# Optimization experiments

Measured on AMD Instinct MI355X. Metric: run time of the kernel, lower is better.

Reference implementation:

```python
import jax, jax.numpy as jnp
import numpy as np

N, D_IN, D_OUT = 128, 512, 512
B = 256

def setup_inputs() -> dict:
    key = jax.random.key(0)
    kx, kw, kb = jax.random.split(key, 3)
    x = jax.random.normal(kx, (B, N, D_IN), dtype=jnp.float32)
    # nn.Linear default init: uniform(-1/sqrt(d_in), 1/sqrt(d_in)) for weight and bias
    bound = 1.0 / np.sqrt(D_IN)
    weight = jax.random.uniform(kw, (N, D_IN, D_OUT), dtype=jnp.float32, minval=-bound, maxval=bound)
    bias = jax.random.uniform(kb, (N, D_OUT), dtype=jnp.float32, minval=-bound, maxval=bound)
    return {"x": x, "weight": weight, "bias": bias}

def reference(x, weight, bias):
    # per-position linear: out[b,n,o] = sum_i x[b,n,i] * W[n,i,o] + bias[n,o]
    out = jnp.einsum('bni,nio->bno', x, weight)
    return out + bias[None]
```

## Files before the change

### kernel.cpp

```cpp
#include <hip/hip_runtime.h>

typedef __attribute__((ext_vector_type(8))) __bf16 bf16x8;
typedef __attribute__((ext_vector_type(4))) float f32x4;

#define DI 512
#define DO 512
#define XROW (128 * DI)
#define OROW (128 * DO)
#define BK 32
#define BUFSZ 24576
#define BOFF  16384

#define VMCNT(n) asm volatile("s_waitcnt vmcnt(" #n ")" ::: "memory")
#define LGKM0()  asm volatile("s_waitcnt lgkmcnt(0)" ::: "memory")
#define SBAR()   __builtin_amdgcn_s_barrier()
#define SCHED0() __builtin_amdgcn_sched_barrier(0)

__global__ __launch_bounds__(512, 4)
void nlinear_mfma(const float* __restrict__ xp, const float* __restrict__ wp,
                  const float* __restrict__ bp, float* __restrict__ op) {
  int blk = blockIdx.x;
  int L = ((blk & 7) << 7) + (blk >> 3);
  int n = L >> 3, mt = (L >> 2) & 1, ot = L & 3;
  int mBase = mt << 7, oBase = ot << 7;

  extern __shared__ char lds[];

  int tid = threadIdx.x, lane = tid & 63, wid = tid >> 6;
  int wm = (wid >> 2) << 6, wn = (wid & 3) << 5;
  int l16 = lane & 15, l4 = lane >> 4;

  unsigned aOff[2];
  #pragma unroll
  for (int i = 0; i < 2; ++i) {
    int r0 = (wid << 4) + (i << 3);
    int row = r0 + (lane >> 3);
    int g = (lane & 7) ^ ((row >> 1) & 7);
    aOff[i] = (unsigned)(((mBase + row) * XROW + n * DI) * 4 + g * 16);
  }

  int bo = tid & 127, bkq = tid >> 7;
  const float* bSrc = wp + ((size_t)n * DI + (bkq << 3)) * DO + oBase + bo;
  int bWrByte = BOFF + bo * 64 + ((bkq ^ ((bo >> 1) & 3)) << 4);

  auto gloadA = [&](int bufOff, int kt) {
    #pragma unroll
    for (int i = 0; i < 2; ++i) {
      int r0 = (wid << 4) + (i << 3);
      __builtin_amdgcn_global_load_lds(
          (const __attribute__((address_space(1))) void*)
              ((const char*)xp + aOff[i] + (unsigned)(kt * 128)),
          (__attribute__((address_space(3))) void*)(lds + bufOff + r0 * 128),
          16, 0, 0);
    }
  };
  auto loadB = [&](int kt, float (&r)[8]) {
    #pragma unroll
    for (int j = 0; j < 8; ++j)
      r[j] = bSrc[(size_t)(kt * BK + j) * DO];
  };
  auto writeB = [&](int bufOff, float (&r)[8]) {
    bf16x8 v;
    #pragma unroll
    for (int j = 0; j < 8; ++j) v[j] = (__bf16)r[j];
    *(bf16x8*)(lds + bufOff + bWrByte) = v;
  };

  f32x4 acc[4][2];
  #pragma unroll
  for (int i = 0; i < 4; ++i)
    #pragma unroll
    for (int j = 0; j < 2; ++j)
      acc[i][j] = f32x4{0.f, 0.f, 0.f, 0.f};

  auto compute = [&](int bufOff) {
    bf16x8 bfr[2];
    #pragma unroll
    for (int j = 0; j < 2; ++j) {
      int row = wn + j * 16 + l16;
      int slot = l4 ^ ((row >> 1) & 3);
      bfr[j] = *(const bf16x8*)(lds + bufOff + BOFF + row * 64 + slot * 16);
    }
    #pragma unroll
    for (int i = 0; i < 4; ++i) {
      int row = wm + i * 16 + l16;
      int v7 = (row >> 1) & 7;
      const char* rb = lds + bufOff + row * 128;
      f32x4 lo = *(const f32x4*)(rb + (((2 * l4) ^ v7) << 4));
      f32x4 hi = *(const f32x4*)(rb + (((2 * l4 + 1) ^ v7) << 4));
      bf16x8 a;
      a[0] = (__bf16)lo.x; a[1] = (__bf16)lo.y; a[2] = (__bf16)lo.z; a[3] = (__bf16)lo.w;
      a[4] = (__bf16)hi.x; a[5] = (__bf16)hi.y; a[6] = (__bf16)hi.z; a[7] = (__bf16)hi.w;
      acc[i][0] = __builtin_amdgcn_mfma_f32_16x16x32_bf16(a, bfr[0], acc[i][0], 0, 0, 0);
      acc[i][1] = __builtin_amdgcn_mfma_f32_16x16x32_bf16(a, bfr[1], acc[i][1], 0, 0, 0);
    }
  };

  float bi[2];
  #pragma unroll
  for (int j = 0; j < 2; ++j)
    bi[j] = bp[n * DO + oBase + wn + j * 16 + l16];

  float bR0[8], bR1[8];
  int cOff = 0, wOff = BUFSZ, gOff = 2 * BUFSZ;

  gloadA(0, 0);
  loadB(0, bR0);
  writeB(0, bR0);
  loadB(1, bR1);
  gloadA(BUFSZ, 1);
  loadB(2, bR0);
  SCHED0();
  LGKM0();
  SBAR();
  SCHED0();

  #define STEP(KT, BRS, VMLINE, DO_LB, DO_GA)                     \
    {                                                             \
      writeB(wOff, BRS);                                          \
      if (DO_GA) gloadA(gOff, (KT) + 2);                          \
      if (DO_LB) loadB((KT) + 3, BRS);                            \
      compute(cOff);                                              \
      SCHED0();                                                   \
      VMLINE;                                                     \
      LGKM0();                                                    \
      SBAR();                                                     \
      SCHED0();                                                   \
      int _t = cOff; cOff = wOff; wOff = gOff; gOff = _t;         \
    }

  for (int kt = 0; kt < 12; kt += 2) {
    STEP(kt,     bR1, VMCNT(18), true, true);
    STEP(kt + 1, bR0, VMCNT(18), true, true);
  }
  STEP(12, bR1, VMCNT(18), true,  true);
  STEP(13, bR0, VMCNT(2),  false, true);
  STEP(14, bR1, VMCNT(0),  false, false);
  compute(cOff);
  #undef STEP

  #pragma unroll
  for (int i = 0; i < 4; ++i) {
    #pragma unroll
    for (int j = 0; j < 2; ++j) {
      #pragma unroll
      for (int r = 0; r < 4; ++r) {
        int m = mBase + wm + i * 16 + l4 * 4 + r;
        int o = oBase + wn + j * 16 + l16;
        op[(size_t)m * OROW + n * DO + o] = acc[i][j][r] + bi[j];
      }
    }
  }
}

extern "C" void kernel_launch(void* const* d_in, const int* in_sizes, int n_in,
                              void* d_out, int out_size, void* d_ws, size_t ws_size,
                              hipStream_t stream) {
  const float* x = (const float*)d_in[0];
  const float* w = (const float*)d_in[1];
  const float* b = (const float*)d_in[2];
  float* o = (float*)d_out;
  hipLaunchKernelGGL(nlinear_mfma, dim3(1024), dim3(512), 3 * BUFSZ, stream,
                     x, w, b, o);
}
```

Baseline: 48.41 us.

## Widen output tile to 128x256 and switch to double-buffered pipeline

Each block now computes a 128x256 output tile instead of 128x128, so the grid halves to 512 blocks and every converted A fragment feeds four MFMAs instead of two. This cuts the redundant reading and fp32-to-bf16 conversion of x across output tiles. The three-stage LDS ring is replaced by a static two-buffer scheme with a simpler loop that prefetches one A tile and two B tiles ahead. The cost is more accumulators and B registers per thread, a shallower pipeline, and fewer blocks, which may hurt occupancy and latency hiding.

```diff
diff --git a/kernel.cpp b/kernel.cpp
--- a/kernel.cpp
+++ b/kernel.cpp
@@ -8,8 +8,8 @@
 #define XROW (128 * DI)
 #define OROW (128 * DO)
 #define BK 32
-#define BUFSZ 24576
-#define BOFF  16384
+#define BOFF 16384
+#define BUFSZ 32768
 
 #define VMCNT(n) asm volatile("s_waitcnt vmcnt(" #n ")" ::: "memory")
 #define LGKM0()  asm volatile("s_waitcnt lgkmcnt(0)" ::: "memory")
@@ -20,14 +20,14 @@
 void nlinear_mfma(const float* __restrict__ xp, const float* __restrict__ wp,
                   const float* __restrict__ bp, float* __restrict__ op) {
   int blk = blockIdx.x;
-  int L = ((blk & 7) << 7) + (blk >> 3);
-  int n = L >> 3, mt = (L >> 2) & 1, ot = L & 3;
-  int mBase = mt << 7, oBase = ot << 7;
+  int L = ((blk & 7) << 6) + (blk >> 3);
+  int n = L >> 2, mt = (L >> 1) & 1, ot = L & 1;
+  int mBase = mt << 7, oBase = ot << 8;
 
-  extern __shared__ char lds[];
+  __shared__ char lds[2 * BUFSZ];
 
   int tid = threadIdx.x, lane = tid & 63, wid = tid >> 6;
-  int wm = (wid >> 2) << 6, wn = (wid & 3) << 5;
+  int wm = (wid >> 2) << 6, wn = (wid & 3) << 6;
   int l16 = lane & 15, l4 = lane >> 4;
 
   unsigned aOff[2];
@@ -38,11 +38,6 @@
     int g = (lane & 7) ^ ((row >> 1) & 7);
     aOff[i] = (unsigned)(((mBase + row) * XROW + n * DI) * 4 + g * 16);
   }
-
-  int bo = tid & 127, bkq = tid >> 7;
-  const float* bSrc = wp + ((size_t)n * DI + (bkq << 3)) * DO + oBase + bo;
-  int bWrByte = BOFF + bo * 64 + ((bkq ^ ((bo >> 1) & 3)) << 4);
-
   auto gloadA = [&](int bufOff, int kt) {
     #pragma unroll
     for (int i = 0; i < 2; ++i) {
@@ -54,95 +49,91 @@
           16, 0, 0);
     }
   };
-  auto loadB = [&](int kt, float (&r)[8]) {
+
+  int bo = tid & 255, kh = tid >> 8;
+  const float* bSrc = wp + ((size_t)n * DI + (kh << 4)) * DO + oBase + bo;
+  int bWr0 = BOFF + bo * 64 + ((((kh << 1))     ^ ((bo >> 1) & 3)) << 4);
+  int bWr1 = BOFF + bo * 64 + ((((kh << 1) | 1) ^ ((bo >> 1) & 3)) << 4);
+
+  float bR[16];
+  auto loadB = [&](int kt) {
     #pragma unroll
-    for (int j = 0; j < 8; ++j)
-      r[j] = bSrc[(size_t)(kt * BK + j) * DO];
+    for (int r = 0; r < 16; ++r)
+      bR[r] = bSrc[(size_t)(kt * BK + r) * DO];
   };
-  auto writeB = [&](int bufOff, float (&r)[8]) {
-    bf16x8 v;
+  auto writeB = [&](int bufOff) {
+    bf16x8 v0, v1;
     #pragma unroll
-    for (int j = 0; j < 8; ++j) v[j] = (__bf16)r[j];
-    *(bf16x8*)(lds + bufOff + bWrByte) = v;
+    for (int r = 0; r < 8; ++r) { v0[r] = (__bf16)bR[r]; v1[r] = (__bf16)bR[8 + r]; }
+    *(bf16x8*)(lds + bufOff + bWr0) = v0;
+    *(bf16x8*)(lds + bufOff + bWr1) = v1;
   };
 
-  f32x4 acc[4][2];
+  f32x4 acc[4][4];
   #pragma unroll
   for (int i = 0; i < 4; ++i)
     #pragma unroll
-    for (int j = 0; j < 2; ++j)
+    for (int j = 0; j < 4; ++j)
       acc[i][j] = f32x4{0.f, 0.f, 0.f, 0.f};
 
   auto compute = [&](int bufOff) {
-    bf16x8 bfr[2];
-    #pragma unroll
-    for (int j = 0; j < 2; ++j) {
-      int row = wn + j * 16 + l16;
-      int slot = l4 ^ ((row >> 1) & 3);
-      bfr[j] = *(const bf16x8*)(lds + bufOff + BOFF + row * 64 + slot * 16);
-    }
+    bf16x8 af[4];
     #pragma unroll
     for (int i = 0; i < 4; ++i) {
       int row = wm + i * 16 + l16;
       int v7 = (row >> 1) & 7;
       const char* rb = lds + bufOff + row * 128;
-      f32x4 lo = *(const f32x4*)(rb + (((2 * l4) ^ v7) << 4));
-      f32x4 hi = *(const f32x4*)(rb + (((2 * l4 + 1) ^ v7) << 4));
-      bf16x8 a;
-      a[0] = (__bf16)lo.x; a[1] = (__bf16)lo.y; a[2] = (__bf16)lo.z; a[3] = (__bf16)lo.w;
-      a[4] = (__bf16)hi.x; a[5] = (__bf16)hi.y; a[6] = (__bf16)hi.z; a[7] = (__bf16)hi.w;
-      acc[i][0] = __builtin_amdgcn_mfma_f32_16x16x32_bf16(a, bfr[0], acc[i][0], 0, 0, 0);
-      acc[i][1] = __builtin_amdgcn_mfma_f32_16x16x32_bf16(a, bfr[1], acc[i][1], 0, 0, 0);
+      f32x4 lo = *(const f32x4*)(rb + ((((l4 << 1))     ^ v7) << 4));
+      f32x4 hi = *(const f32x4*)(rb + ((((l4 << 1) | 1) ^ v7) << 4));
+      af[i][0] = (__bf16)lo.x; af[i][1] = (__bf16)lo.y;
+      af[i][2] = (__bf16)lo.z; af[i][3] = (__bf16)lo.w;
+      af[i][4] = (__bf16)hi.x; af[i][5] = (__bf16)hi.y;
+      af[i][6] = (__bf16)hi.z; af[i][7] = (__bf16)hi.w;
+    }
+    #pragma unroll
+    for (int j = 0; j < 4; ++j) {
+      int row = wn + j * 16 + l16;
+      int slot = l4 ^ ((row >> 1) & 3);
+      bf16x8 bfr = *(const bf16x8*)(lds + bufOff + BOFF + row * 64 + slot * 16);
+      #pragma unroll
+      for (int i = 0; i < 4; ++i)
+        acc[i][j] = __builtin_amdgcn_mfma_f32_16x16x32_bf16(af[i], bfr, acc[i][j], 0, 0, 0);
     }
   };
 
-  float bi[2];
+  float bi[4];
   #pragma unroll
-  for (int j = 0; j < 2; ++j)
+  for (int j = 0; j < 4; ++j)
     bi[j] = bp[n * DO + oBase + wn + j * 16 + l16];
 
-  float bR0[8], bR1[8];
-  int cOff = 0, wOff = BUFSZ, gOff = 2 * BUFSZ;
+  gloadA(0, 0);
+  loadB(0);
+  writeB(0);
+  loadB(1);
+  SCHED0(); LGKM0(); SBAR(); SCHED0();
 
-  gloadA(0, 0);
-  loadB(0, bR0);
-  writeB(0, bR0);
-  loadB(1, bR1);
-  gloadA(BUFSZ, 1);
-  loadB(2, bR0);
+  for (int kt = 0; kt < 14; ++kt) {
+    int curOff = (kt & 1) * BUFSZ, nxtOff = curOff ^ BUFSZ;
+    writeB(nxtOff);
+    gloadA(nxtOff, kt + 1);
+    loadB(kt + 2);
+    compute(curOff);
+    SCHED0();
+    VMCNT(16);
+    LGKM0(); SBAR(); SCHED0();
+  }
+  writeB(BUFSZ);
+  gloadA(BUFSZ, 15);
+  compute(0);
   SCHED0();
-  LGKM0();
-  SBAR();
-  SCHED0();
-
-  #define STEP(KT, BRS, VMLINE, DO_LB, DO_GA)                     \
-    {                                                             \
-      writeB(wOff, BRS);                                          \
-      if (DO_GA) gloadA(gOff, (KT) + 2);                          \
-      if (DO_LB) loadB((KT) + 3, BRS);                            \
-      compute(cOff);                                              \
-      SCHED0();                                                   \
-      VMLINE;                                                     \
-      LGKM0();                                                    \
-      SBAR();                                                     \
-      SCHED0();                                                   \
-      int _t = cOff; cOff = wOff; wOff = gOff; gOff = _t;         \
-    }
-
-  for (int kt = 0; kt < 12; kt += 2) {
-    STEP(kt,     bR1, VMCNT(18), true, true);
-    STEP(kt + 1, bR0, VMCNT(18), true, true);
-  }
-  STEP(12, bR1, VMCNT(18), true,  true);
-  STEP(13, bR0, VMCNT(2),  false, true);
-  STEP(14, bR1, VMCNT(0),  false, false);
-  compute(cOff);
-  #undef STEP
+  VMCNT(0);
+  LGKM0(); SBAR(); SCHED0();
+  compute(BUFSZ);
 
   #pragma unroll
   for (int i = 0; i < 4; ++i) {
     #pragma unroll
-    for (int j = 0; j < 2; ++j) {
+    for (int j = 0; j < 4; ++j) {
       #pragma unroll
       for (int r = 0; r < 4; ++r) {
         int m = mBase + wm + i * 16 + l4 * 4 + r;
@@ -160,6 +151,5 @@
   const float* w = (const float*)d_in[1];
   const float* b = (const float*)d_in[2];
   float* o = (float*)d_out;
-  hipLaunchKernelGGL(nlinear_mfma, dim3(1024), dim3(512), 3 * BUFSZ, stream,
-                     x, w, b, o);
+  hipLaunchKernelGGL(nlinear_mfma, dim3(512), dim3(512), 0, stream, x, w, b, o);
 }
```

Result: no change. 48.03 us (-0.8%).
